# Performance work log

Hardware: AMD Instinct MI355X
Metric: run time of the kernel (lower is better)

The kernel has to match this reference:

```python
import jax, jax.numpy as jnp
import numpy as np

ITERATIONS = 20


def _affine_sample(canvas, theta):
    """PyTorch-equivalent F.affine_grid + F.grid_sample (bilinear,
    align_corners=False, padding_mode='zeros') for all T transforms at once.
    canvas: [H, W], theta: [T, 2, 3] -> returns [T, H, W].
    """
    H, W = canvas.shape
    dt = canvas.dtype
    # Normalized base grid coords, align_corners=False: centers of pixels.
    xs = (jnp.arange(W, dtype=dt) * 2 + 1) / W - 1  # [W]
    ys = (jnp.arange(H, dtype=dt) * 2 + 1) / H - 1  # [H]
    # Sampled normalized coords: [x', y'] = theta @ [x, y, 1]
    gx = (theta[:, 0, 0, None, None] * xs[None, None, :]
          + theta[:, 0, 1, None, None] * ys[None, :, None]
          + theta[:, 0, 2, None, None])  # [T, H, W]
    gy = (theta[:, 1, 0, None, None] * xs[None, None, :]
          + theta[:, 1, 1, None, None] * ys[None, :, None]
          + theta[:, 1, 2, None, None])  # [T, H, W]
    # Unnormalize to pixel coords (align_corners=False).
    ix = (gx + 1) * (W * 0.5) - 0.5
    iy = (gy + 1) * (H * 0.5) - 0.5
    x0f = jnp.floor(ix)
    y0f = jnp.floor(iy)
    wx1 = ix - x0f
    wy1 = iy - y0f
    wx0 = 1 - wx1
    wy0 = 1 - wy1
    x0 = x0f.astype(jnp.int32)
    y0 = y0f.astype(jnp.int32)

    def corner(xi, yi):
        valid = (xi >= 0) & (xi < W) & (yi >= 0) & (yi < H)
        v = canvas[jnp.clip(yi, 0, H - 1), jnp.clip(xi, 0, W - 1)]
        return jnp.where(valid, v, jnp.zeros((), dt))  # zeros padding

    return (wx0 * wy0 * corner(x0, y0)
            + wx1 * wy0 * corner(x0 + 1, y0)
            + wx0 * wy1 * corner(x0, y0 + 1)
            + wx1 * wy1 * corner(x0 + 1, y0 + 1))


def setup_inputs() -> dict:
    key = jax.random.key(0)
    k1, k2, k3 = jax.random.split(key, 3)
    H, W, T = 1024, 1024, 16
    canvas0 = jax.random.uniform(k1, (H, W), dtype=jnp.float32)
    theta = jax.random.normal(k2, (T, 2, 3), dtype=jnp.float32)
    probs = jax.random.uniform(k3, (T,), dtype=jnp.float32)
    base_value = jnp.zeros((1,), dtype=jnp.float32)
    return {"canvas0": canvas0, "theta": theta, "probs": probs,
            "base_value": base_value}


def reference(canvas0, theta, probs, base_value):
    p = probs / jnp.sum(probs)

    def step(canvas, _):
        sampled = _affine_sample(canvas, theta)          # [T, H, W]
        new_canvas = jnp.einsum('t,thw->hw', p, sampled)  # weighted IFS sum
        return new_canvas, None

    canvas, _ = jax.lax.scan(step, canvas0, None, length=ITERATIONS)
    return canvas + base_value[0]
```

## Files before the change

kernel.cpp:

```cpp
#include <hip/hip_runtime.h>

constexpr int W = 1024;
constexpr int H = 1024;
constexpr int T = 16;
constexpr int ITERS = 20;
constexpr int PITCH = 1040;
constexpr int PH = H + 2;
constexpr int PAD_ELEMS = PH * PITCH;
constexpr int TILES_X = W / 16;
constexpr int TILES_Y = H / 16;

typedef float f2 __attribute__((ext_vector_type(2), aligned(4)));

__global__ void setup_coef(const float* __restrict__ theta,
                           const float* __restrict__ probs,
                           float* __restrict__ coef) {
    int t = threadIdx.x;
    if (t >= T) return;
    float sum = 0.f;
    for (int i = 0; i < T; ++i) sum += probs[i];
    float p = probs[t] / sum;
    const float* th = theta + 6 * t;
    float a = th[0], b = th[1], c = th[2];
    float d = th[3], e = th[4], f = th[5];
    float Cx = a * ((1.0f - (float)W) * 0.5f)
             + b * ((1.0f - (float)H) * 0.5f)
             + (c + 1.0f) * ((float)W * 0.5f) - 0.5f;
    float Cy = d * ((1.0f - (float)W) * 0.5f)
             + e * ((1.0f - (float)H) * 0.5f)
             + (f + 1.0f) * ((float)H * 0.5f) - 0.5f;
    float* o = coef + 8 * t;
    o[0] = p;  o[1] = a;  o[2] = b;  o[3] = Cx + 1.0f;
    o[4] = d;  o[5] = e;  o[6] = Cy + 1.0f; o[7] = 0.f;
}

__global__ __launch_bounds__(256) void setup_mask(const float* __restrict__ coef,
                                                  unsigned* __restrict__ mask) {
    int tile = blockIdx.x * 256 + threadIdx.x;
    if (tile >= TILES_X * TILES_Y) return;
    int tx = tile & (TILES_X - 1), ty = tile / TILES_X;
    float w0 = (float)(tx * 16), w1 = w0 + 15.f;
    float h0 = (float)(ty * 16), h1 = h0 + 15.f;
    unsigned m = 0;
    for (int t = 0; t < T; ++t) {
        float Ax = coef[t * 8 + 1], Bx = coef[t * 8 + 2], Cx = coef[t * 8 + 3];
        float Ay = coef[t * 8 + 4], By = coef[t * 8 + 5], Cy = coef[t * 8 + 6];
        float ixmin = Cx + (Ax >= 0.f ? Ax * w0 : Ax * w1) + (Bx >= 0.f ? Bx * h0 : Bx * h1);
        float ixmax = Cx + (Ax >= 0.f ? Ax * w1 : Ax * w0) + (Bx >= 0.f ? Bx * h1 : Bx * h0);
        float iymin = Cy + (Ay >= 0.f ? Ay * w0 : Ay * w1) + (By >= 0.f ? By * h0 : By * h1);
        float iymax = Cy + (Ay >= 0.f ? Ay * w1 : Ay * w0) + (By >= 0.f ? By * h1 : By * h0);
        bool hit = !(ixmax <= 0.f || ixmin >= (float)(W + 1) ||
                     iymax <= 0.f || iymin >= (float)(H + 1));
        if (hit) m |= (1u << t);
    }
    mask[tile] = m;
}

__global__ __launch_bounds__(256) void copy_in(const float* __restrict__ src,
                                               float* __restrict__ dst) {
    int i = blockIdx.x * 256 + threadIdx.x;
    int h = i >> 10, w = i & 1023;
    dst[(h + 1) * PITCH + (w + 1)] = src[i];
}

__global__ __launch_bounds__(256) void ifs_iter(const float* __restrict__ in,
                                                float* __restrict__ out,
                                                const float* __restrict__ coef,
                                                const unsigned* __restrict__ mask,
                                                const float* __restrict__ base,
                                                int dstPitch, int dstOff,
                                                int add_base) {
    __shared__ float sc[(T + 3) * 8];

    unsigned tmask = mask[blockIdx.y * TILES_X + blockIdx.x];
    int nact = __popc(tmask);
    int lid = threadIdx.x;

    if (lid < T * 8) {
        int t = lid >> 3;
        if (tmask & (1u << t)) {
            int pos = __popc(tmask & ((1u << t) - 1));
            sc[pos * 8 + (lid & 7)] = coef[lid];
        }
    }
    if (lid < 24) sc[nact * 8 + lid] = 0.f;
    __syncthreads();

    int lane = lid & 63;
    int wv   = lid >> 6;
    int w = blockIdx.x * 16 + ((wv & 1) << 3) + (lane & 7);
    int h = blockIdx.y * 16 + ((wv >> 1) << 3) + (lane >> 3);
    float wf = (float)w, hf = (float)h;

    float acc = 0.f;

    for (int g = 0; g < nact; g += 4) {
        const float* c = sc + g * 8;
        float fx[4], fy[4], pe[4];
        int id0[4];
#pragma unroll
        for (int k = 0; k < 4; ++k) {
            const float* ck = c + k * 8;
            float p = ck[0], Ax = ck[1], Bx = ck[2], Cx = ck[3];
            float Ay = ck[4], By = ck[5], Cy = ck[6];
            float x = fmaf(Ax, wf, fmaf(Bx, hf, Cx));
            float y = fmaf(Ay, wf, fmaf(By, hf, Cy));
            float xf = floorf(x), yf = floorf(y);
            bool act = (xf >= 0.f) & (xf <= (float)W) & (yf >= 0.f) & (yf <= (float)H);
            id0[k] = act ? (int)fmaf(yf, (float)PITCH, xf) : 0;
            pe[k]  = act ? p : 0.f;
            fx[k] = x - xf;
            fy[k] = y - yf;
        }
        f2 r0[4], r1[4];
#pragma unroll
        for (int k = 0; k < 4; ++k) {
            r0[k] = *(const f2*)(in + id0[k]);
            r1[k] = *(const f2*)(in + id0[k] + PITCH);
        }
#pragma unroll
        for (int k = 0; k < 4; ++k) {
            float top = fmaf(fx[k], r0[k].y - r0[k].x, r0[k].x);
            float bot = fmaf(fx[k], r1[k].y - r1[k].x, r1[k].x);
            acc = fmaf(pe[k], fmaf(fy[k], bot - top, top), acc);
        }
    }

    if (add_base) acc += base[0];
    out[h * dstPitch + w + dstOff] = acc;
}

extern "C" void kernel_launch(void* const* d_in, const int* in_sizes, int n_in,
                              void* d_out, int out_size, void* d_ws, size_t ws_size,
                              hipStream_t stream) {
    const float* canvas0 = (const float*)d_in[0];
    const float* theta   = (const float*)d_in[1];
    const float* probs   = (const float*)d_in[2];
    const float* base    = (const float*)d_in[3];
    float* out = (float*)d_out;

    float* bufA = (float*)d_ws;
    float* bufB = bufA + PAD_ELEMS;
    float* coef = bufB + PAD_ELEMS;
    unsigned* mask = (unsigned*)(coef + T * 8);

    hipMemsetAsync(d_ws, 0, (size_t)2 * PAD_ELEMS * sizeof(float), stream);

    setup_coef<<<1, 64, 0, stream>>>(theta, probs, coef);
    setup_mask<<<(TILES_X * TILES_Y + 255) / 256, 256, 0, stream>>>(coef, mask);
    copy_in<<<(H * W) / 256, 256, 0, stream>>>(canvas0, bufA);

    dim3 block(256);
    dim3 grid(TILES_X, TILES_Y);

    const float* cur = bufA;
    for (int i = 0; i < ITERS; ++i) {
        bool last = (i == ITERS - 1);
        float* dst = last ? out : ((i & 1) ? bufA : bufB);
        int dstPitch = last ? W : PITCH;
        int dstOff   = last ? 0 : (PITCH + 1);
        ifs_iter<<<grid, block, 0, stream>>>(cur, dst, coef, mask, base,
                                             dstPitch, dstOff, last ? 1 : 0);
        cur = dst;
    }
}
```

Baseline: 418.7 us.

## Precompute per-tile compacted transform tables and clamp coordinates into a zero border

```diff
diff --git a/kernel.cpp b/kernel.cpp
--- a/kernel.cpp
+++ b/kernel.cpp
@@ -6,9 +6,11 @@
 constexpr int ITERS = 20;
 constexpr int PITCH = 1040;
 constexpr int PH = H + 2;
-constexpr int PAD_ELEMS = PH * PITCH;
+constexpr int GROWS = PH + 2;
+constexpr int ALLOC = 16 + GROWS * PITCH;
 constexpr int TILES_X = W / 16;
 constexpr int TILES_Y = H / 16;
+constexpr int NTILES = TILES_X * TILES_Y;
 
 typedef float f2 __attribute__((ext_vector_type(2), aligned(4)));
 
@@ -30,30 +32,39 @@
              + e * ((1.0f - (float)H) * 0.5f)
              + (f + 1.0f) * ((float)H * 0.5f) - 0.5f;
     float* o = coef + 8 * t;
-    o[0] = p;  o[1] = a;  o[2] = b;  o[3] = Cx + 1.0f;
-    o[4] = d;  o[5] = e;  o[6] = Cy + 1.0f; o[7] = 0.f;
+    o[0] = p;  o[1] = a;  o[2] = b;  o[3] = Cx + 2.0f;
+    o[4] = d;  o[5] = e;  o[6] = Cy + 2.0f; o[7] = 0.f;
 }
 
-__global__ __launch_bounds__(256) void setup_mask(const float* __restrict__ coef,
-                                                  unsigned* __restrict__ mask) {
+__global__ __launch_bounds__(256) void setup_tiles(const float* __restrict__ coef,
+                                                   float* __restrict__ tbl,
+                                                   int* __restrict__ tcnt) {
     int tile = blockIdx.x * 256 + threadIdx.x;
-    if (tile >= TILES_X * TILES_Y) return;
-    int tx = tile & (TILES_X - 1), ty = tile / TILES_X;
+    if (tile >= NTILES) return;
+    int tx = tile & (TILES_X - 1), ty = tile >> 6;
     float w0 = (float)(tx * 16), w1 = w0 + 15.f;
     float h0 = (float)(ty * 16), h1 = h0 + 15.f;
-    unsigned m = 0;
+    float* o = tbl + tile * 128;
+    int n = 0;
     for (int t = 0; t < T; ++t) {
-        float Ax = coef[t * 8 + 1], Bx = coef[t * 8 + 2], Cx = coef[t * 8 + 3];
-        float Ay = coef[t * 8 + 4], By = coef[t * 8 + 5], Cy = coef[t * 8 + 6];
-        float ixmin = Cx + (Ax >= 0.f ? Ax * w0 : Ax * w1) + (Bx >= 0.f ? Bx * h0 : Bx * h1);
-        float ixmax = Cx + (Ax >= 0.f ? Ax * w1 : Ax * w0) + (Bx >= 0.f ? Bx * h1 : Bx * h0);
-        float iymin = Cy + (Ay >= 0.f ? Ay * w0 : Ay * w1) + (By >= 0.f ? By * h0 : By * h1);
-        float iymax = Cy + (Ay >= 0.f ? Ay * w1 : Ay * w0) + (By >= 0.f ? By * h1 : By * h0);
-        bool hit = !(ixmax <= 0.f || ixmin >= (float)(W + 1) ||
-                     iymax <= 0.f || iymin >= (float)(H + 1));
-        if (hit) m |= (1u << t);
+        const float* c = coef + t * 8;
+        float Ax = c[1], Bx = c[2], Cx = c[3];
+        float Ay = c[4], By = c[5], Cy = c[6];
+        float xmin = Cx + (Ax >= 0.f ? Ax * w0 : Ax * w1) + (Bx >= 0.f ? Bx * h0 : Bx * h1);
+        float xmax = Cx + (Ax >= 0.f ? Ax * w1 : Ax * w0) + (Bx >= 0.f ? Bx * h1 : Bx * h0);
+        float ymin = Cy + (Ay >= 0.f ? Ay * w0 : Ay * w1) + (By >= 0.f ? By * h0 : By * h1);
+        float ymax = Cy + (Ay >= 0.f ? Ay * w1 : Ay * w0) + (By >= 0.f ? By * h1 : By * h0);
+        bool hit = !(xmax <= 1.f || xmin >= (float)(W + 2) ||
+                     ymax <= 1.f || ymin >= (float)(H + 2));
+        if (hit) {
+            for (int j = 0; j < 8; ++j) o[n * 8 + j] = c[j];
+            ++n;
+        }
     }
-    mask[tile] = m;
+    tcnt[tile] = n;
+    int np = (n + 3) & ~3;
+    for (int s = n; s < np; ++s)
+        for (int j = 0; j < 8; ++j) o[s * 8 + j] = 0.f;
 }
 
 __global__ __launch_bounds__(256) void copy_in(const float* __restrict__ src,
@@ -63,68 +74,63 @@
     dst[(h + 1) * PITCH + (w + 1)] = src[i];
 }
 
+template <int K>
+__device__ __forceinline__ void ifs_body(const float* __restrict__ tc, int g,
+                                         const float* __restrict__ gb,
+                                         float wf, float hf, float& acc) {
+    float fx[K], fy[K], pp[K];
+    int off[K];
+#pragma unroll
+    for (int k = 0; k < K; ++k) {
+        const float* c = tc + (g + k) * 8;
+        float p = c[0], Ax = c[1], Bx = c[2], Cx = c[3];
+        float Ay = c[4], By = c[5], Cy = c[6];
+        float xb = fmaf(Ax, wf, fmaf(Bx, hf, Cx));
+        float yb = fmaf(Ay, wf, fmaf(By, hf, Cy));
+        xb = fminf(fmaxf(xb, 0.f), 1037.f);
+        yb = fminf(fmaxf(yb, 0.f), 1026.f);
+        float xi = floorf(xb), yi = floorf(yb);
+        fx[k] = xb - xi;
+        fy[k] = yb - yi;
+        off[k] = (int)fmaf(yi, (float)PITCH, xi);
+        pp[k] = p;
+    }
+    f2 r0[K], r1[K];
+#pragma unroll
+    for (int k = 0; k < K; ++k) {
+        r0[k] = *(const f2*)(gb + off[k]);
+        r1[k] = *(const f2*)(gb + off[k] + PITCH);
+    }
+#pragma unroll
+    for (int k = 0; k < K; ++k) {
+        float top = fmaf(fx[k], r0[k].y - r0[k].x, r0[k].x);
+        float bot = fmaf(fx[k], r1[k].y - r1[k].x, r1[k].x);
+        acc = fmaf(pp[k], fmaf(fy[k], bot - top, top), acc);
+    }
+}
+
 __global__ __launch_bounds__(256) void ifs_iter(const float* __restrict__ in,
                                                 float* __restrict__ out,
-                                                const float* __restrict__ coef,
-                                                const unsigned* __restrict__ mask,
+                                                const float* __restrict__ tbl,
+                                                const int* __restrict__ tcnt,
                                                 const float* __restrict__ base,
                                                 int dstPitch, int dstOff,
                                                 int add_base) {
-    __shared__ float sc[(T + 3) * 8];
+    int tile = blockIdx.y * TILES_X + blockIdx.x;
+    const float* tc = tbl + tile * 128;
+    int np = (tcnt[tile] + 3) & ~3;
 
-    unsigned tmask = mask[blockIdx.y * TILES_X + blockIdx.x];
-    int nact = __popc(tmask);
     int lid = threadIdx.x;
-
-    if (lid < T * 8) {
-        int t = lid >> 3;
-        if (tmask & (1u << t)) {
-            int pos = __popc(tmask & ((1u << t) - 1));
-            sc[pos * 8 + (lid & 7)] = coef[lid];
-        }
-    }
-    if (lid < 24) sc[nact * 8 + lid] = 0.f;
-    __syncthreads();
-
-    int lane = lid & 63;
-    int wv   = lid >> 6;
-    int w = blockIdx.x * 16 + ((wv & 1) << 3) + (lane & 7);
-    int h = blockIdx.y * 16 + ((wv >> 1) << 3) + (lane >> 3);
+    int lane = lid & 63, wv = lid >> 6;
+    int w = (blockIdx.x << 4) + ((wv & 1) << 3) + (lane & 7);
+    int h = (blockIdx.y << 4) + ((wv >> 1) << 3) + (lane >> 3);
     float wf = (float)w, hf = (float)h;
+    const float* gb = in - (PITCH + 1);
 
     float acc = 0.f;
-
-    for (int g = 0; g < nact; g += 4) {
-        const float* c = sc + g * 8;
-        float fx[4], fy[4], pe[4];
-        int id0[4];
-#pragma unroll
-        for (int k = 0; k < 4; ++k) {
-            const float* ck = c + k * 8;
-            float p = ck[0], Ax = ck[1], Bx = ck[2], Cx = ck[3];
-            float Ay = ck[4], By = ck[5], Cy = ck[6];
-            float x = fmaf(Ax, wf, fmaf(Bx, hf, Cx));
-            float y = fmaf(Ay, wf, fmaf(By, hf, Cy));
-            float xf = floorf(x), yf = floorf(y);
-            bool act = (xf >= 0.f) & (xf <= (float)W) & (yf >= 0.f) & (yf <= (float)H);
-            id0[k] = act ? (int)fmaf(yf, (float)PITCH, xf) : 0;
-            pe[k]  = act ? p : 0.f;
-            fx[k] = x - xf;
-            fy[k] = y - yf;
-        }
-        f2 r0[4], r1[4];
-#pragma unroll
-        for (int k = 0; k < 4; ++k) {
-            r0[k] = *(const f2*)(in + id0[k]);
-            r1[k] = *(const f2*)(in + id0[k] + PITCH);
-        }
-#pragma unroll
-        for (int k = 0; k < 4; ++k) {
-            float top = fmaf(fx[k], r0[k].y - r0[k].x, r0[k].x);
-            float bot = fmaf(fx[k], r1[k].y - r1[k].x, r1[k].x);
-            acc = fmaf(pe[k], fmaf(fy[k], bot - top, top), acc);
-        }
-    }
+    int g = 0;
+    for (; g + 8 <= np; g += 8) ifs_body<8>(tc, g, gb, wf, hf, acc);
+    if (g < np)                 ifs_body<4>(tc, g, gb, wf, hf, acc);
 
     if (add_base) acc += base[0];
     out[h * dstPitch + w + dstOff] = acc;
@@ -137,17 +143,18 @@
     const float* theta   = (const float*)d_in[1];
     const float* probs   = (const float*)d_in[2];
     const float* base    = (const float*)d_in[3];
-    float* out = (float*)d_out;
 
-    float* bufA = (float*)d_ws;
-    float* bufB = bufA + PAD_ELEMS;
-    float* coef = bufB + PAD_ELEMS;
-    unsigned* mask = (unsigned*)(coef + T * 8);
+    float* raw  = (float*)d_ws;
+    float* bufA = raw + 16 + PITCH;
+    float* bufB = raw + ALLOC + 16 + PITCH;
+    float* coef = raw + 2 * ALLOC;
+    float* tbl  = coef + T * 8;
+    int*   tcnt = (int*)(tbl + NTILES * 128);
 
-    hipMemsetAsync(d_ws, 0, (size_t)2 * PAD_ELEMS * sizeof(float), stream);
+    hipMemsetAsync(raw, 0, (size_t)2 * ALLOC * sizeof(float), stream);
 
     setup_coef<<<1, 64, 0, stream>>>(theta, probs, coef);
-    setup_mask<<<(TILES_X * TILES_Y + 255) / 256, 256, 0, stream>>>(coef, mask);
+    setup_tiles<<<(NTILES + 255) / 256, 256, 0, stream>>>(coef, tbl, tcnt);
     copy_in<<<(H * W) / 256, 256, 0, stream>>>(canvas0, bufA);
 
     dim3 block(256);
@@ -156,10 +163,10 @@
     const float* cur = bufA;
     for (int i = 0; i < ITERS; ++i) {
         bool last = (i == ITERS - 1);
-        float* dst = last ? out : ((i & 1) ? bufA : bufB);
+        float* dst = last ? (float*)d_out : ((i & 1) ? bufA : bufB);
         int dstPitch = last ? W : PITCH;
         int dstOff   = last ? 0 : (PITCH + 1);
-        ifs_iter<<<grid, block, 0, stream>>>(cur, dst, coef, mask, base,
+        ifs_iter<<<grid, block, 0, stream>>>(cur, dst, tbl, tcnt, base,
                                              dstPitch, dstOff, last ? 1 : 0);
         cur = dst;
     }
```

After: 416.0 us. Within noise of the previous version (-0.6%).
